# Performance work log

Measured on AMD Instinct MI355X. Metric: run time of the kernel, lower is better.

Reference implementation:

```python
import jax, jax.numpy as jnp
import numpy as np

CA, CZ, CS, CSI = 128, 128, 384, 256
NH, HD, NB, A = 8, 16, 6, 7
RMAX, SMAX = 32, 2
RELP_DIM = 4 * (RMAX + 1) + 1 + 2 * (SMAX + 1)  # 139


def make_relp(L):
    # single-chain relative-position features: [L, L, 139]
    i = jnp.arange(L)
    d = i[:, None] - i[None, :]
    a_rel_pos = jax.nn.one_hot(jnp.clip(d + RMAX, 0, 2 * RMAX), 2 * (RMAX + 1))
    d_tok = jnp.where(d == 0, RMAX, 2 * RMAX + 1)  # same-res only on diagonal
    a_rel_tok = jax.nn.one_hot(d_tok, 2 * (RMAX + 1))
    same_ent = jnp.ones((L, L, 1), jnp.float32)
    a_rel_chain = jax.nn.one_hot(jnp.full((L, L), SMAX), 2 * (SMAX + 1))
    return jnp.concatenate([a_rel_pos, a_rel_tok, same_ent, a_rel_chain], axis=-1)


def ln(x, g, b):
    m = x.mean(-1, keepdims=True)
    v = ((x - m) ** 2).mean(-1, keepdims=True)
    return (x - m) / jnp.sqrt(v + 1e-5) * g + b


def setup_inputs():
    key = jax.random.key(0)
    ks = iter(jax.random.split(key, 64))
    def p(*shape):
        return (jax.random.normal(next(ks), shape, jnp.float32) * 0.05)
    B, Ns, L = 1, 2, 384
    inp = dict(
        x_t=jax.random.normal(next(ks), (B, Ns, L, A, 3), jnp.float32),
        sigma=jax.random.uniform(next(ks), (B, Ns), jnp.float32),
        s_inputs=jax.random.normal(next(ks), (B, L, CSI), jnp.float32),
        s_trunk=jax.random.normal(next(ks), (B, L, CS), jnp.float32),
        z_trunk=jax.random.normal(next(ks), (B, L, L, CZ), jnp.float32),
        token_mask=jnp.ones((B, L), bool),
        s_in_w=p(CSI, CS), s_in_b=p(CS),
        relp_w=p(RELP_DIM, CZ), relp_b=p(CZ),
        t1_w=p(1, CS), t1_b=p(CS), t2_w=p(CS, CS), t2_b=p(CS),
        xp_w=p(3 * A, CA), xp_b=p(CA),
        s2a_w=p(CS, CA), s2a_b=p(CA),
        out_w=p(CA, 3 * A), out_b=p(3 * A),
        an_g=jnp.ones((NB, CA)), an_b=jnp.zeros((NB, CA)),
        zn_g=jnp.ones((NB, CZ)), zn_b=jnp.zeros((NB, CZ)),
        qw=p(NB, CA, CA), qb=p(NB, CA),
        kw=p(NB, CA, CA), kb=p(NB, CA),
        vw=p(NB, CA, CA), vb=p(NB, CA),
        zw=p(NB, CZ, NH), zb=p(NB, NH),
        ow=p(NB, CA, CA), ob=p(NB, CA),
        f1w=p(NB, CA, 4 * CA), f1b=p(NB, 4 * CA),
        f2w=p(NB, 4 * CA, CA), f2b=p(NB, CA),
    )
    return inp


def reference(x_t, sigma, s_inputs, s_trunk, z_trunk, token_mask,
              s_in_w, s_in_b, relp_w, relp_b, t1_w, t1_b, t2_w, t2_b,
              xp_w, xp_b, s2a_w, s2a_b, out_w, out_b,
              an_g, an_b, zn_g, zn_b, qw, qb, kw, kb, vw, vb,
              zw, zb, ow, ob, f1w, f1b, f2w, f2b):
    B, Ns, L = x_t.shape[:3]
    relp = make_relp(L)                                   # [L, L, 139]
    pair_z = z_trunk + relp @ relp_w + relp_b             # [B, L, L, CZ]
    s_cond = s_trunk + s_inputs @ s_in_w + s_in_b         # [B, L, CS]
    t_feat = jax.nn.silu(sigma.reshape(B * Ns, 1) @ t1_w + t1_b) @ t2_w + t2_b
    single_s = s_cond[:, None] + t_feat.reshape(B, Ns, CS)[:, :, None]  # [B,Ns,L,CS]
    a = x_t.reshape(B, Ns, L, 3 * A) @ xp_w + xp_b + single_s @ s2a_w + s2a_b
    a2 = a.reshape(B * Ns, L, CA)
    z2 = jnp.broadcast_to(pair_z[:, None], (B, Ns, L, L, CZ)).reshape(B * Ns, L, L, CZ)
    m = jnp.broadcast_to(token_mask[:, None], (B, Ns, L)).reshape(B * Ns, L)
    pair_mask = m[:, :, None] & m[:, None, :]             # [B*Ns, L, L]
    scale = 1.0 / np.sqrt(HD).astype(np.float32)
    for i in range(NB):
        an = ln(a2, an_g[i], an_b[i])
        zn = ln(z2, zn_g[i], zn_b[i])
        q = (an @ qw[i] + qb[i]).reshape(-1, L, NH, HD)
        k = (an @ kw[i] + kb[i]).reshape(-1, L, NH, HD)
        v = (an @ vw[i] + vb[i]).reshape(-1, L, NH, HD)
        logits = jnp.einsum('blhd,bmhd->bhlm', q, k) * scale
        bias = (zn @ zw[i] + zb[i]).transpose(0, 3, 1, 2)  # [B*Ns, NH, L, L]
        logits = jnp.where(pair_mask[:, None], logits + bias, -1e9)
        attn = jax.nn.softmax(logits, axis=-1)
        o = jnp.einsum('bhlm,bmhd->blhd', attn, v).reshape(-1, L, CA)
        a2 = a2 + (o @ ow[i] + ob[i])
        an2 = ln(a2, an_g[i], an_b[i])
        a2 = a2 + jax.nn.gelu(an2 @ f1w[i] + f1b[i], approximate=False) @ f2w[i] + f2b[i]
    vout = (a2 @ out_w + out_b).reshape(B, Ns, L, A, 3)
    return vout * token_mask[:, None, :, None, None].astype(vout.dtype)
```

## Files before the change

### kernel.cpp

```cpp
#include <hip/hip_runtime.h>
#include <math.h>

#define L 384
#define CA 128
#define NH 8
#define HD 16
#define NB 6
#define NS 2
#define NP (L*L)

typedef __attribute__((ext_vector_type(4))) float f32x4;
typedef __attribute__((ext_vector_type(8))) short s16x8;
typedef __attribute__((ext_vector_type(4))) unsigned short u16x4;
typedef unsigned short ushort_t;

__device__ inline unsigned short f2bf(float f){
  union { float f; unsigned int u; } v; v.f = f;
  unsigned int u = v.u;
  unsigned int r = u + 0x7FFF + ((u>>16)&1);
  return (unsigned short)(r>>16);
}
__device__ inline float bf2f(ushort_t u){
  union { float f; unsigned int i; } v; v.i = ((unsigned int)u)<<16; return v.f;
}

#define WT_LAYER 196608

__global__ __launch_bounds__(256) void k_pre0(
    const float* zng, const float* znb, const float* zw, const float* zb,
    const float* relp_w, const float* relp_b,
    ushort_t* wzT, float* rbase, float* cb){
  int t = threadIdx.x;
  __shared__ float part[48][5];
  for(int idx=t; idx<6144; idx+=256){
    int h = idx>>7, c = idx&127;
    wzT[h*128+c] = f2bf(zng[(h>>3)*128+c]*zw[((h>>3)*128+c)*8+(h&7)]);
  }
  if(t<128) rbase[t] = relp_w[132*128+t] + relp_w[135*128+t] + relp_b[t];
  if(t<192){
    int h = t>>2, ch = t&3, blk = h>>3, hh = h&7;
    float acc = 0.f;
    #pragma unroll 8
    for(int c=ch*32; c<ch*32+32; c++)
      acc += znb[blk*128+c]*zw[(blk*128+c)*8+hh];
    part[h][ch] = acc;
  }
  __syncthreads();
  if(t<48) cb[t] = zb[t] + part[t][0]+part[t][1]+part[t][2]+part[t][3];
}

__global__ __launch_bounds__(256, 4) void k_mega(
    const float* z_trunk, const float* relp_w, const float* rbase,
    const ushort_t* wzT, const float* cb, ushort_t* bias_all,
    const float* qw, const float* kw, const float* vw,
    const float* f1w, const float* f2w, const float* ow,
    const float* s_in_w, const float* s2a_w,
    ushort_t* wT, ushort_t* s_in_wT, ushort_t* s2a_wT,
    const float* sigma, const float* t1w, const float* t1b,
    const float* t2w, const float* t2b, float* t_feat){
  __shared__ float smem[4160];
  int bid = blockIdx.x, t = threadIdx.x;

  if(bid < 2304){
    int lane = t&63, wv = t>>6;
    int rowf = lane&15, kg = lane>>4;
    int p0 = bid*64 + wv*16;
    int p = p0 + rowf;
    int i = p/L, j = p - i*L, d = i - j;
    int r1 = d+32; r1 = r1<0?0:(r1>64?64:r1);
    int r2 = (d==0) ? 98 : 131;
    const float* zp  = z_trunk + (size_t)p*128 + kg*8;

    f32x4 z0a = *(const f32x4*)(zp+  0), z0b = *(const f32x4*)(zp+  4);
    f32x4 z1a = *(const f32x4*)(zp+ 32), z1b = *(const f32x4*)(zp+ 36);
    f32x4 z2a = *(const f32x4*)(zp+ 64), z2b = *(const f32x4*)(zp+ 68);
    f32x4 z3a = *(const f32x4*)(zp+ 96), z3b = *(const f32x4*)(zp+100);

    const float* w1p = relp_w + r1*128 + kg*8;
    const float* w2p = relp_w + r2*128 + kg*8;
    const float* rbp = rbase + kg*8;
    f32x4 c0a = *(const f32x4*)(w1p+  0) + *(const f32x4*)(w2p+  0) + *(const f32x4*)(rbp+  0);
    f32x4 c0b = *(const f32x4*)(w1p+  4) + *(const f32x4*)(w2p+  4) + *(const f32x4*)(rbp+  4);
    f32x4 c1a = *(const f32x4*)(w1p+ 32) + *(const f32x4*)(w2p+ 32) + *(const f32x4*)(rbp+ 32);
    f32x4 c1b = *(const f32x4*)(w1p+ 36) + *(const f32x4*)(w2p+ 36) + *(const f32x4*)(rbp+ 36);
    f32x4 c2a = *(const f32x4*)(w1p+ 64) + *(const f32x4*)(w2p+ 64) + *(const f32x4*)(rbp+ 64);
    f32x4 c2b = *(const f32x4*)(w1p+ 68) + *(const f32x4*)(w2p+ 68) + *(const f32x4*)(rbp+ 68);
    f32x4 c3a = *(const f32x4*)(w1p+ 96) + *(const f32x4*)(w2p+ 96) + *(const f32x4*)(rbp+ 96);
    f32x4 c3b = *(const f32x4*)(w1p+100) + *(const f32x4*)(w2p+100) + *(const f32x4*)(rbp+100);

    float val[4][8];
    float s = 0.f;
    #pragma unroll
    for(int jj=0;jj<4;jj++){
      val[0][jj]   = z0a[jj]+c0a[jj];  val[0][jj+4] = z0b[jj]+c0b[jj];
      val[1][jj]   = z1a[jj]+c1a[jj];  val[1][jj+4] = z1b[jj]+c1b[jj];
      val[2][jj]   = z2a[jj]+c2a[jj];  val[2][jj+4] = z2b[jj]+c2b[jj];
      val[3][jj]   = z3a[jj]+c3a[jj];  val[3][jj+4] = z3b[jj]+c3b[jj];
    }
    #pragma unroll
    for(int ks=0;ks<4;ks++)
      #pragma unroll
      for(int jj=0;jj<8;jj++) s += val[ks][jj];
    s += __shfl_xor(s,16,64); s += __shfl_xor(s,32,64);
    float mean = s*(1.f/128.f);
    float q2 = 0.f;
    #pragma unroll
    for(int ks=0; ks<4; ks++)
      #pragma unroll
      for(int jj=0;jj<8;jj++){ float dd = val[ks][jj]-mean; q2 += dd*dd; }
    q2 += __shfl_xor(q2,16,64); q2 += __shfl_xor(q2,32,64);
    float rstd = rsqrtf(q2*(1.f/128.f) + 1e-5f);

    s16x8 af[4];
    #pragma unroll
    for(int ks=0; ks<4; ks++)
      #pragma unroll
      for(int jj=0;jj<8;jj++) af[ks][jj] = (short)f2bf((val[ks][jj]-mean)*rstd);

    float* myc = smem + wv*816;
    #pragma unroll
    for(int ht=0; ht<3; ht++){
      int col = ht*16 + rowf;
      float cbv = cb[col];
      f32x4 acc = {cbv,cbv,cbv,cbv};
      #pragma unroll
      for(int ks=0; ks<4; ks++){
        s16x8 bf = *(const s16x8*)&wzT[col*128 + ks*32 + kg*8];
        acc = __builtin_amdgcn_mfma_f32_16x16x32_bf16(af[ks], bf, acc, 0,0,0);
      }
      #pragma unroll
      for(int i2=0;i2<4;i2++) myc[col*17 + kg*4 + i2] = acc[i2];
    }
    int i0 = p0/L, qt_ = i0>>4, q16 = i0&15, j0 = p0 - i0*L;
    #pragma unroll
    for(int it=0; it<12; it++){
      int idx = lane + it*64;
      int pl = idx>>4, c = idx&15;
      int li_ = pl>>3, h_ = pl&7;
      bias_all[(size_t)((li_*24+qt_)*8+h_)*6144 + q16*384 + j0 + c] =
          f2bf(myc[pl*17 + c]);
    }
  } else if(bid < 2628){
    float (*tl)[65] = (float(*)[65])smem;
    int b = bid - 2304;
    const float* src; ushort_t* dst;
    int M, N, k0, n0;
    if(b < 96){
      int mat = b>>2, li = mat>>2, wsel = mat&3, tile = b&3;
      const float* const ws_[4] = {qw, kw, vw, ow};
      const int off_[4] = {0, 16384, 32768, 180224};
      src = ws_[wsel] + (size_t)li*16384;
      dst = wT + (size_t)li*WT_LAYER + off_[wsel];
      M = 128; N = 128; k0 = (tile>>1)*64; n0 = (tile&1)*64;
    } else if(b < 192){
      int idx = b-96, li = idx>>4, tile = idx&15;
      src = f1w + (size_t)li*65536;
      dst = wT + (size_t)li*WT_LAYER + 49152;
      M = 128; N = 512; k0 = (tile>>3)*64; n0 = (tile&7)*64;
    } else if(b < 288){
      int idx = b-192, li = idx>>4, tile = idx&15;
      src = f2w + (size_t)li*65536;
      dst = wT + (size_t)li*WT_LAYER + 114688;
      M = 512; N = 128; k0 = (tile>>1)*64; n0 = (tile&1)*64;
    } else if(b < 312){
      int tile = b-288;
      src = s_in_w; dst = s_in_wT;
      M = 256; N = 384; k0 = (tile/6)*64; n0 = (tile%6)*64;
    } else {
      int tile = b-312;
      src = s2a_w; dst = s2a_wT;
      M = 384; N = 128; k0 = (tile>>1)*64; n0 = (tile&1)*64;
    }
    float v[16];
    #pragma unroll
    for(int it=0;it<16;it++){
      int i = t + it*256;
      v[it] = src[(size_t)(k0+(i>>6))*N + n0+(i&63)];
    }
    #pragma unroll
    for(int it=0;it<16;it++){
      int i = t + it*256;
      tl[i>>6][i&63] = v[it];
    }
    __syncthreads();
    #pragma unroll
    for(int it=0;it<16;it++){
      int i = t + it*256;
      dst[(size_t)(n0+(i>>6))*M + k0+(i&63)] = f2bf(tl[i&63][i>>6]);
    }
  } else {
    int j = bid - 2628;
    int s = j/6, c0 = (j%6)*64;
    float sg = sigma[s];
    for(int i=t; i<384; i+=256){
      float x = sg*t1w[i] + t1b[i];
      smem[i] = x / (1.f + expf(-x));
    }
    __syncthreads();
    int col = c0 + (t&63), ch = t>>6;
    float acc = 0.f;
    #pragma unroll 8
    for(int k=ch*96; k<ch*96+96; k++)
      acc += smem[k]*t2w[(size_t)k*384+col];
    smem[384 + ch*64 + (t&63)] = acc;
    __syncthreads();
    if(t<64)
      t_feat[s*384 + c0 + t] = t2b[c0+t]
        + smem[384+t] + smem[448+t] + smem[512+t] + smem[576+t];
  }
}

__device__ inline void qkv_project(ushort_t zh[16][152], const ushort_t* wTl,
                                   const float* qb, const float* kb, const float* vb,
                                   ushort_t* q_bf, ushort_t* k_bf, ushort_t* vT_bf,
                                   int s_idx, int lbase, int wv, int rowf, int kg){
  s16x8 af[4];
  #pragma unroll
  for(int ks=0;ks<4;ks++) af[ks] = *(const s16x8*)&zh[rowf][ks*32 + kg*8];
  #pragma unroll
  for(int u=0;u<6;u++){
    int unit = wv*6 + u;
    int proj = unit>>3, nt = unit&7;
    int col = nt*16 + rowf;
    const ushort_t* wp = wTl + proj*16384;
    const float* bias = proj==0? qb : (proj==1? kb : vb);
    float bv = bias[col];
    f32x4 acc = {bv,bv,bv,bv};
    #pragma unroll
    for(int ks=0;ks<4;ks++){
      s16x8 bf = *(const s16x8*)&wp[col*128 + ks*32 + kg*8];
      acc = __builtin_amdgcn_mfma_f32_16x16x32_bf16(af[ks], bf, acc, 0,0,0);
    }
    int sh = s_idx*NH + nt;
    if(proj==2){
      #pragma unroll
      for(int i2=0;i2<4;i2++)
        vT_bf[((size_t)sh*16 + rowf)*384 + lbase + kg*4 + i2] = f2bf(acc[i2]);
    } else {
      float sc = (proj==0)? 0.25f : 1.0f;
      ushort_t* outp = (proj==0)? q_bf : k_bf;
      #pragma unroll
      for(int i2=0;i2<4;i2++)
        outp[((size_t)sh*384 + lbase + kg*4 + i2)*16 + rowf] = f2bf(acc[i2]*sc);
    }
  }
}

__global__ __launch_bounds__(256) void k_qkv0(
    const float* x_t, const float* s_inputs, const float* s_trunk,
    const float* s_in_b, const ushort_t* s_in_wT,
    const float* s2a_b, const ushort_t* s2a_wT,
    const float* xp_w, const float* xp_b, const float* t_feat,
    const float* g, const float* bb,
    const ushort_t* wTl, const float* qb, const float* kb, const float* vb,
    float* a2, ushort_t* q_bf, ushort_t* k_bf, ushort_t* vT_bf){
  __shared__ ushort_t si[16][280];
  __shared__ ushort_t scb[16][408];
  __shared__ float xrow[16][21];
  __shared__ float a_new[16][132];
  __shared__ ushort_t zh[16][152];
  int t = threadIdx.x, lane = t&63, wv = t>>6;
  int rowf = lane&15, kg = lane>>4;
  int bid = blockIdx.x, s_idx = bid/24, lt = bid%24;
  int lr0 = lt*16;

  for(int i=t;i<16*256;i+=256){
    int r=i>>8, c=i&255;
    si[r][c] = f2bf(s_inputs[(size_t)(lr0+r)*256+c]);
  }
  for(int i=t;i<16*21;i+=256){
    int r=i/21, u=i%21;
    xrow[r][u] = x_t[((size_t)s_idx*L + lr0 + r)*21 + u];
  }
  __syncthreads();

  {
    s16x8 af1[8];
    #pragma unroll
    for(int ks=0;ks<8;ks++) af1[ks] = *(const s16x8*)&si[rowf][ks*32+kg*8];
    const float* tf = t_feat + s_idx*384;
    #pragma unroll
    for(int nn=0;nn<6;nn++){
      int col = (wv*6+nn)*16 + rowf;
      float bv = s_in_b[col];
      f32x4 acc = {bv,bv,bv,bv};
      #pragma unroll
      for(int ks=0;ks<8;ks++){
        s16x8 bf = *(const s16x8*)&s_in_wT[col*256 + ks*32 + kg*8];
        acc = __builtin_amdgcn_mfma_f32_16x16x32_bf16(af1[ks], bf, acc, 0,0,0);
      }
      float tfc = tf[col];
      #pragma unroll
      for(int i2=0;i2<4;i2++){
        int r = kg*4+i2;
        scb[r][col] = f2bf(acc[i2] + s_trunk[(size_t)(lr0+r)*384+col] + tfc);
      }
    }
  }
  __syncthreads();

  {
    s16x8 xf[12];
    #pragma unroll
    for(int ks=0;ks<12;ks++) xf[ks] = *(const s16x8*)&scb[rowf][ks*32+kg*8];
    #pragma unroll
    for(int nn=0;nn<2;nn++){
      int col = (wv*2+nn)*16 + rowf;
      float base = xp_b[col] + s2a_b[col];
      f32x4 acc;
      #pragma unroll
      for(int i2=0;i2<4;i2++){
        float xc = base;
        #pragma unroll
        for(int u=0;u<21;u++) xc += xrow[kg*4+i2][u]*xp_w[u*128+col];
        acc[i2] = xc;
      }
      #pragma unroll
      for(int ks=0;ks<12;ks++){
        s16x8 bf = *(const s16x8*)&s2a_wT[col*384 + ks*32 + kg*8];
        acc = __builtin_amdgcn_mfma_f32_16x16x32_bf16(xf[ks], bf, acc, 0,0,0);
      }
      #pragma unroll
      for(int i2=0;i2<4;i2++){
        int r = kg*4+i2;
        a_new[r][col] = acc[i2];
        a2[((size_t)(s_idx*L + lr0 + r))*128 + col] = acc[i2];
      }
    }
  }
  __syncthreads();

  {
    int row = t>>4, sub = t&15;
    const float* xp = &a_new[row][sub*8];
    f32x4 x0 = *(const f32x4*)xp;
    f32x4 x1 = *(const f32x4*)(xp+4);
    float s = x0[0]+x0[1]+x0[2]+x0[3]+x1[0]+x1[1]+x1[2]+x1[3];
    s += __shfl_xor(s,1,64); s += __shfl_xor(s,2,64);
    s += __shfl_xor(s,4,64); s += __shfl_xor(s,8,64);
    float mean = s*(1.f/128.f);
    float q2 = 0.f;
    #pragma unroll
    for(int jj=0;jj<4;jj++){ float d0=x0[jj]-mean, d1=x1[jj]-mean; q2 += d0*d0+d1*d1; }
    q2 += __shfl_xor(q2,1,64); q2 += __shfl_xor(q2,2,64);
    q2 += __shfl_xor(q2,4,64); q2 += __shfl_xor(q2,8,64);
    float rstd = rsqrtf(q2*(1.f/128.f)+1e-5f);
    int c0 = sub*8;
    f32x4 g0 = *(const f32x4*)(g+c0), g1 = *(const f32x4*)(g+c0+4);
    f32x4 b0 = *(const f32x4*)(bb+c0), b1 = *(const f32x4*)(bb+c0+4);
    s16x8 pack;
    #pragma unroll
    for(int jj=0;jj<4;jj++){
      pack[jj]   = (short)f2bf((x0[jj]-mean)*rstd*g0[jj]+b0[jj]);
      pack[jj+4] = (short)f2bf((x1[jj]-mean)*rstd*g1[jj]+b1[jj]);
    }
    *(s16x8*)&zh[row][c0] = pack;
  }
  __syncthreads();
  qkv_project(zh, wTl, qb, kb, vb, q_bf, k_bf, vT_bf, s_idx, lr0, wv, rowf, kg);
}

__global__ __launch_bounds__(1024) void k_fused(
    float* a2, const float* an_g, const float* an_b, const ushort_t* wT,
    const float* qb_all, const float* kb_all, const float* vb_all,
    const float* ob_all, const float* f1b_all, const float* f2b_all,
    ushort_t* q_bf, ushort_t* k_bf, ushort_t* vT_bf,
    const ushort_t* bias_all, const float* out_w, const float* out_b,
    float* out, int li){
  __shared__ float orow[16][132];
  __shared__ float ocomb[8][16][20];
  __shared__ float lcomb[8][16];
  union SM {
    struct {
      ushort_t biasw[16][16][200];
      ushort_t P[16][16][72];
    } fl;
    struct {
      float a_new[16][132];
      ushort_t zh[16][152];
      ushort_t h_lds[16][536];
      float fcomb[8][16][20];
    } post;
  };
  __shared__ SM sm;

  int t = threadIdx.x, lane = t&63, wv = t>>6;
  int rowf = lane&15, kg = lane>>4;
  int bid = blockIdx.x, s_idx = bid/24, qt = bid%24;
  int r0 = bid*16;
  const ushort_t* wTl = wT + (size_t)li*WT_LAYER;
  const float* g  = an_g + li*128;
  const float* bb = an_b + li*128;

  {
    int h = wv>>1, kh = wv&1;
    int sh = s_idx*NH + h;
    {
      const ushort_t* btile = bias_all + (size_t)(li*24+qt)*8*6144
                            + (size_t)h*16*384 + kh*192;
      #pragma unroll
      for(int it=0; it<6; it++){
        int idx = lane + it*64;
        int row = idx/24, seg = idx%24;
        *(s16x8*)&sm.fl.biasw[wv][row][seg*8] =
            *(const s16x8*)&btile[(size_t)row*384 + seg*8];
      }
    }
    ushort_t (*Pw)[72] = sm.fl.P[wv];
    s16x8 qf = {0,0,0,0,0,0,0,0};
    if(kg < 2) qf = *(const s16x8*)&q_bf[((size_t)sh*384 + qt*16 + rowf)*16 + kg*8];
    const ushort_t* kp = k_bf + (size_t)sh*384*16;
    const ushort_t* vp = vT_bf + ((size_t)sh*16 + rowf)*384;

    f32x4 o0 = {0,0,0,0}, o1 = {0,0,0,0};
    float l_acc = 0.f;

    s16x8 kfc[4];
    #pragma unroll
    for(int t4=0;t4<4;t4++){
      kfc[t4] = (s16x8){0,0,0,0,0,0,0,0};
      if(kg < 2) kfc[t4] = *(const s16x8*)&kp[((size_t)(kh*192 + t4*16 + rowf))*16 + kg*8];
    }

    #pragma unroll
    for(int c=0;c<3;c++){
      int key0 = kh*192 + c*64;
      s16x8 vbf0 = *(const s16x8*)&vp[key0 + kg*8];
      s16x8 vbf1 = *(const s16x8*)&vp[key0 + 32 + kg*8];
      s16x8 kfn[4];
      if(c < 2){
        #pragma unroll
        for(int t4=0;t4<4;t4++){
          kfn[t4] = (s16x8){0,0,0,0,0,0,0,0};
          if(kg < 2) kfn[t4] = *(const s16x8*)&kp[((size_t)(key0 + 64 + t4*16 + rowf))*16 + kg*8];
        }
      }
      f32x4 st[4];
      #pragma unroll
      for(int t4=0;t4<4;t4++){
        u16x4 bb4 = *(const u16x4*)&sm.fl.biasw[wv][rowf][c*64 + t4*16 + kg*4];
        f32x4 cin;
        #pragma unroll
        for(int jj=0;jj<4;jj++) cin[jj] = bf2f(bb4[jj]);
        st[t4] = __builtin_amdgcn_mfma_f32_16x16x32_bf16(kfc[t4], qf, cin, 0,0,0);
      }
      #pragma unroll
      for(int t4=0;t4<4;t4++){
        float p0 = __expf(st[t4][0]), p1 = __expf(st[t4][1]);
        float p2 = __expf(st[t4][2]), p3 = __expf(st[t4][3]);
        l_acc += (p0+p1)+(p2+p3);
        u16x4 pk = {f2bf(p0), f2bf(p1), f2bf(p2), f2bf(p3)};
        *(u16x4*)&Pw[rowf][t4*16 + kg*4] = pk;
      }
      {
        s16x8 pa = *(const s16x8*)&Pw[rowf][kg*8];
        o0 = __builtin_amdgcn_mfma_f32_16x16x32_bf16(pa, vbf0, o0, 0,0,0);
        s16x8 pb = *(const s16x8*)&Pw[rowf][32 + kg*8];
        o1 = __builtin_amdgcn_mfma_f32_16x16x32_bf16(pb, vbf1, o1, 0,0,0);
      }
      if(c < 2){
        #pragma unroll
        for(int t4=0;t4<4;t4++) kfc[t4] = kfn[t4];
      }
    }
    f32x4 o_acc = o0 + o1;
    l_acc += __shfl_xor(l_acc, 16, 64);
    l_acc += __shfl_xor(l_acc, 32, 64);
    if(kh==1){
      #pragma unroll
      for(int i2=0;i2<4;i2++) ocomb[h][kg*4+i2][rowf] = o_acc[i2];
      if(kg==0) lcomb[h][rowf] = l_acc;
    }
    __syncthreads();
    if(kh==0){
      l_acc += lcomb[h][rowf];
      #pragma unroll
      for(int i2=0;i2<4;i2++) o_acc[i2] += ocomb[h][kg*4+i2][rowf];
      float inv = 1.f / l_acc;
      #pragma unroll
      for(int i2=0;i2<4;i2++){
        float invq = __shfl(inv, kg*4 + i2, 64);
        orow[kg*4+i2][h*16 + rowf] = o_acc[i2]*invq;
      }
    }
  }
  __syncthreads();

  if(wv < 8){
    s16x8 af[4];
    #pragma unroll
    for(int ks=0;ks<4;ks++){
      f32x4 v0 = *(const f32x4*)&orow[rowf][ks*32+kg*8];
      f32x4 v1 = *(const f32x4*)&orow[rowf][ks*32+kg*8+4];
      s16x8 p;
      #pragma unroll
      for(int jj=0;jj<4;jj++){ p[jj] = (short)f2bf(v0[jj]); p[jj+4] = (short)f2bf(v1[jj]); }
      af[ks] = p;
    }
    const ushort_t* wo = wTl + 180224;
    const float* obp = ob_all + li*128;
    int col = wv*16 + rowf;
    float bv = obp[col];
    f32x4 acc = {bv,bv,bv,bv};
    f32x4 accB = {0,0,0,0};
    #pragma unroll
    for(int ks=0;ks<2;ks++){
      s16x8 bf = *(const s16x8*)&wo[col*128 + ks*32 + kg*8];
      acc = __builtin_amdgcn_mfma_f32_16x16x32_bf16(af[ks], bf, acc, 0,0,0);
      s16x8 bf2 = *(const s16x8*)&wo[col*128 + (ks+2)*32 + kg*8];
      accB = __builtin_amdgcn_mfma_f32_16x16x32_bf16(af[ks+2], bf2, accB, 0,0,0);
    }
    acc += accB;
    #pragma unroll
    for(int i2=0;i2<4;i2++){
      int r = kg*4+i2;
      sm.post.a_new[r][col] = a2[(size_t)(r0+r)*128 + col] + acc[i2];
    }
  }
  __syncthreads();

  {
    int row = wv, c0 = lane*2;
    float x0 = sm.post.a_new[row][c0], x1 = sm.post.a_new[row][c0+1];
    float s = x0+x1;
    s += __shfl_xor(s,1,64); s += __shfl_xor(s,2,64); s += __shfl_xor(s,4,64);
    s += __shfl_xor(s,8,64); s += __shfl_xor(s,16,64); s += __shfl_xor(s,32,64);
    float mean = s*(1.f/128.f);
    float d0=x0-mean, d1=x1-mean;
    float q2 = d0*d0+d1*d1;
    q2 += __shfl_xor(q2,1,64); q2 += __shfl_xor(q2,2,64); q2 += __shfl_xor(q2,4,64);
    q2 += __shfl_xor(q2,8,64); q2 += __shfl_xor(q2,16,64); q2 += __shfl_xor(q2,32,64);
    float rstd = rsqrtf(q2*(1.f/128.f)+1e-5f);
    unsigned int pk = (unsigned int)f2bf(d0*rstd*g[c0]+bb[c0])
                    | ((unsigned int)f2bf(d1*rstd*g[c0+1]+bb[c0+1])<<16);
    *(unsigned int*)&sm.post.zh[row][c0] = pk;
  }
  __syncthreads();

  {
    s16x8 xf[4];
    #pragma unroll
    for(int ks=0;ks<4;ks++) xf[ks] = *(const s16x8*)&sm.post.zh[rowf][ks*32 + kg*8];
    const ushort_t* w1 = wTl + 49152;
    const float* f1bp = f1b_all + li*512;
    #pragma unroll
    for(int nn=0; nn<2; nn++){
      int col = (wv*2+nn)*16 + rowf;
      float bv = f1bp[col];
      f32x4 acc = {bv,bv,bv,bv};
      #pragma unroll
      for(int ks=0;ks<4;ks++){
        s16x8 bf = *(const s16x8*)&w1[col*128 + ks*32 + kg*8];
        acc = __builtin_amdgcn_mfma_f32_16x16x32_bf16(xf[ks], bf, acc, 0,0,0);
      }
      #pragma unroll
      for(int i2=0;i2<4;i2++){
        float x = acc[i2];
        float ge = 0.5f*x*(1.f + erff(x*0.70710678f));
        sm.post.h_lds[kg*4+i2][col] = f2bf(ge);
      }
    }
  }
  __syncthreads();

  {
    const ushort_t* w2 = wTl + 114688;
    const float* f2bp = f2b_all + li*128;
    int ct = wv>>1, kh2 = wv&1;
    int col2 = ct*16 + rowf;
    float bv = kh2? 0.f : f2bp[col2];
    f32x4 accA = {bv,bv,bv,bv};
    f32x4 accB = {0,0,0,0};
    int ks0 = kh2*8;
    #pragma unroll
    for(int kk=0; kk<4; kk++){
      s16x8 hfA = *(const s16x8*)&sm.post.h_lds[rowf][(ks0+kk)*32 + kg*8];
      s16x8 bfA = *(const s16x8*)&w2[col2*512 + (ks0+kk)*32 + kg*8];
      accA = __builtin_amdgcn_mfma_f32_16x16x32_bf16(hfA, bfA, accA, 0,0,0);
      s16x8 hfB = *(const s16x8*)&sm.post.h_lds[rowf][(ks0+kk+4)*32 + kg*8];
      s16x8 bfB = *(const s16x8*)&w2[col2*512 + (ks0+kk+4)*32 + kg*8];
      accB = __builtin_amdgcn_mfma_f32_16x16x32_bf16(hfB, bfB, accB, 0,0,0);
    }
    accA += accB;
    if(kh2==1){
      #pragma unroll
      for(int i2=0;i2<4;i2++) sm.post.fcomb[ct][kg*4+i2][rowf] = accA[i2];
    }
    __syncthreads();
    if(kh2==0){
      #pragma unroll
      for(int i2=0;i2<4;i2++){
        int r = kg*4+i2;
        float fin = sm.post.a_new[r][col2] + accA[i2] + sm.post.fcomb[ct][r][rowf];
        a2[(size_t)(r0+r)*128 + col2] = fin;
        sm.post.a_new[r][col2] = fin;
      }
    }
  }
  __syncthreads();

  if(li < NB-1){
    const float* g2  = an_g + (li+1)*128;
    const float* bb2 = an_b + (li+1)*128;
    {
      int row = wv, c0 = lane*2;
      float x0 = sm.post.a_new[row][c0], x1 = sm.post.a_new[row][c0+1];
      float s = x0+x1;
      s += __shfl_xor(s,1,64); s += __shfl_xor(s,2,64); s += __shfl_xor(s,4,64);
      s += __shfl_xor(s,8,64); s += __shfl_xor(s,16,64); s += __shfl_xor(s,32,64);
      float mean = s*(1.f/128.f);
      float d0=x0-mean, d1=x1-mean;
      float q2 = d0*d0+d1*d1;
      q2 += __shfl_xor(q2,1,64); q2 += __shfl_xor(q2,2,64); q2 += __shfl_xor(q2,4,64);
      q2 += __shfl_xor(q2,8,64); q2 += __shfl_xor(q2,16,64); q2 += __shfl_xor(q2,32,64);
      float rstd = rsqrtf(q2*(1.f/128.f)+1e-5f);
      unsigned int pk = (unsigned int)f2bf(d0*rstd*g2[c0]+bb2[c0])
                      | ((unsigned int)f2bf(d1*rstd*g2[c0+1]+bb2[c0+1])<<16);
      *(unsigned int*)&sm.post.zh[row][c0] = pk;
    }
    __syncthreads();
    {
      const ushort_t* wTn = wT + (size_t)(li+1)*WT_LAYER;
      const float* qb2 = qb_all + (li+1)*128;
      const float* kb2 = kb_all + (li+1)*128;
      const float* vb2 = vb_all + (li+1)*128;
      s16x8 af[4];
      #pragma unroll
      for(int ks=0;ks<4;ks++) af[ks] = *(const s16x8*)&sm.post.zh[rowf][ks*32 + kg*8];
      #pragma unroll
      for(int u=0;u<2;u++){
        int unit = wv + u*16;
        if(unit < 24){
          int proj = unit>>3, nt = unit&7;
          int col = nt*16 + rowf;
          const ushort_t* wp = wTn + proj*16384;
          const float* bias = proj==0? qb2 : (proj==1? kb2 : vb2);
          float bv = bias[col];
          f32x4 acc = {bv,bv,bv,bv};
          #pragma unroll
          for(int ks=0;ks<4;ks++){
            s16x8 bf = *(const s16x8*)&wp[col*128 + ks*32 + kg*8];
            acc = __builtin_amdgcn_mfma_f32_16x16x32_bf16(af[ks], bf, acc, 0,0,0);
          }
          int sh = s_idx*NH + nt;
          if(proj==2){
            #pragma unroll
            for(int i2=0;i2<4;i2++)
              vT_bf[((size_t)sh*16 + rowf)*384 + qt*16 + kg*4 + i2] = f2bf(acc[i2]);
          } else {
            float sc = (proj==0)? 0.25f : 1.0f;
            ushort_t* outp = (proj==0)? q_bf : k_bf;
            #pragma unroll
            for(int i2=0;i2<4;i2++)
              outp[((size_t)sh*384 + qt*16 + kg*4 + i2)*16 + rowf] = f2bf(acc[i2]*sc);
          }
        }
      }
    }
  } else {
    for(int idx=t; idx<336; idx+=1024){
      int r = idx/21, c = idx%21;
      float acc = out_b[c];
      #pragma unroll 8
      for(int kk=0;kk<128;kk++) acc += sm.post.a_new[r][kk]*out_w[kk*21+c];
      out[(size_t)(r0+r)*21 + c] = acc;
    }
  }
}

extern "C" void kernel_launch(void* const* d_in, const int* in_sizes, int n_in,
                              void* d_out, int out_size, void* d_ws, size_t ws_size,
                              hipStream_t stream){
  const float* x_t      = (const float*)d_in[0];
  const float* sigma    = (const float*)d_in[1];
  const float* s_inputs = (const float*)d_in[2];
  const float* s_trunk  = (const float*)d_in[3];
  const float* z_trunk  = (const float*)d_in[4];
  const float* s_in_w = (const float*)d_in[6];
  const float* s_in_b = (const float*)d_in[7];
  const float* relp_w = (const float*)d_in[8];
  const float* relp_b = (const float*)d_in[9];
  const float* t1_w = (const float*)d_in[10];
  const float* t1_b = (const float*)d_in[11];
  const float* t2_w = (const float*)d_in[12];
  const float* t2_b = (const float*)d_in[13];
  const float* xp_w = (const float*)d_in[14];
  const float* xp_b = (const float*)d_in[15];
  const float* s2a_w = (const float*)d_in[16];
  const float* s2a_b = (const float*)d_in[17];
  const float* out_w = (const float*)d_in[18];
  const float* out_b = (const float*)d_in[19];
  const float* an_g = (const float*)d_in[20];
  const float* an_b = (const float*)d_in[21];
  const float* zn_g = (const float*)d_in[22];
  const float* zn_b = (const float*)d_in[23];
  const float* qw = (const float*)d_in[24];
  const float* qb = (const float*)d_in[25];
  const float* kw = (const float*)d_in[26];
  const float* kb = (const float*)d_in[27];
  const float* vw = (const float*)d_in[28];
  const float* vb = (const float*)d_in[29];
  const float* zw = (const float*)d_in[30];
  const float* zb = (const float*)d_in[31];
  const float* ow = (const float*)d_in[32];
  const float* ob = (const float*)d_in[33];
  const float* f1w = (const float*)d_in[34];
  const float* f1b = (const float*)d_in[35];
  const float* f2w = (const float*)d_in[36];
  const float* f2b = (const float*)d_in[37];

  float* ws = (float*)d_ws;
  ushort_t* bias_all = (ushort_t*)ws;
  float* cb     = ws + (size_t)24*NP;
  float* t_feat = cb + 48;
  float* a2     = t_feat + 768;
  float* rbase  = a2 + (size_t)NS*L*CA;
  ushort_t* wT      = (ushort_t*)(rbase + 128);
  ushort_t* wzT     = wT + (size_t)6*WT_LAYER;
  ushort_t* q_bf    = wzT + 6144;
  ushort_t* k_bf    = q_bf + 98304;
  ushort_t* vT_bf   = k_bf + 98304;
  ushort_t* s_in_wT = vT_bf + 98304;
  ushort_t* s2a_wT  = s_in_wT + 98304;
  float* outp = (float*)d_out;

  k_pre0<<<1,256,0,stream>>>(zn_g,zn_b,zw,zb,relp_w,relp_b,wzT,rbase,cb);
  k_mega<<<2640,256,0,stream>>>(z_trunk,relp_w,rbase,wzT,cb,bias_all,
                                qw,kw,vw,f1w,f2w,ow,s_in_w,s2a_w,
                                wT,s_in_wT,s2a_wT,
                                sigma,t1_w,t1_b,t2_w,t2_b,t_feat);
  k_qkv0<<<48,256,0,stream>>>(x_t,s_inputs,s_trunk,s_in_b,s_in_wT,
                              s2a_b,s2a_wT,xp_w,xp_b,t_feat,
                              an_g, an_b, wT, qb, kb, vb,
                              a2, q_bf, k_bf, vT_bf);
  for(int i=0;i<NB;i++){
    k_fused<<<48,1024,0,stream>>>(a2, an_g, an_b, wT,
        qb, kb, vb, ob, f1b, f2b,
        q_bf, k_bf, vT_bf, bias_all,
        out_w, out_b, outp, i);
  }
}
```

Measured before the change: 198.8 us.

## Reorder mega-kernel blocks and prefetch weight fragments ahead of barriers

The mega kernel now dispatches the weight-transpose and time-embedding blocks first, so these short latency-bound tasks are not queued behind the 2304 pair-bias blocks. The time-embedding work is split across twice as many blocks to spread out its dependent loop. In the fused layer kernel, the out-projection, FFN1, FFN2 and next-layer QKV weight fragments are loaded into registers before the preceding __syncthreads, so global load latency overlaps the barrier wait, and some barriers are removed or moved. The cost is higher register pressure in a 1024-thread block, which may cause spills.

```diff
diff --git a/kernel.cpp b/kernel.cpp
--- a/kernel.cpp
+++ b/kernel.cpp
@@ -61,88 +61,9 @@
   __shared__ float smem[4160];
   int bid = blockIdx.x, t = threadIdx.x;
 
-  if(bid < 2304){
-    int lane = t&63, wv = t>>6;
-    int rowf = lane&15, kg = lane>>4;
-    int p0 = bid*64 + wv*16;
-    int p = p0 + rowf;
-    int i = p/L, j = p - i*L, d = i - j;
-    int r1 = d+32; r1 = r1<0?0:(r1>64?64:r1);
-    int r2 = (d==0) ? 98 : 131;
-    const float* zp  = z_trunk + (size_t)p*128 + kg*8;
-
-    f32x4 z0a = *(const f32x4*)(zp+  0), z0b = *(const f32x4*)(zp+  4);
-    f32x4 z1a = *(const f32x4*)(zp+ 32), z1b = *(const f32x4*)(zp+ 36);
-    f32x4 z2a = *(const f32x4*)(zp+ 64), z2b = *(const f32x4*)(zp+ 68);
-    f32x4 z3a = *(const f32x4*)(zp+ 96), z3b = *(const f32x4*)(zp+100);
-
-    const float* w1p = relp_w + r1*128 + kg*8;
-    const float* w2p = relp_w + r2*128 + kg*8;
-    const float* rbp = rbase + kg*8;
-    f32x4 c0a = *(const f32x4*)(w1p+  0) + *(const f32x4*)(w2p+  0) + *(const f32x4*)(rbp+  0);
-    f32x4 c0b = *(const f32x4*)(w1p+  4) + *(const f32x4*)(w2p+  4) + *(const f32x4*)(rbp+  4);
-    f32x4 c1a = *(const f32x4*)(w1p+ 32) + *(const f32x4*)(w2p+ 32) + *(const f32x4*)(rbp+ 32);
-    f32x4 c1b = *(const f32x4*)(w1p+ 36) + *(const f32x4*)(w2p+ 36) + *(const f32x4*)(rbp+ 36);
-    f32x4 c2a = *(const f32x4*)(w1p+ 64) + *(const f32x4*)(w2p+ 64) + *(const f32x4*)(rbp+ 64);
-    f32x4 c2b = *(const f32x4*)(w1p+ 68) + *(const f32x4*)(w2p+ 68) + *(const f32x4*)(rbp+ 68);
-    f32x4 c3a = *(const f32x4*)(w1p+ 96) + *(const f32x4*)(w2p+ 96) + *(const f32x4*)(rbp+ 96);
-    f32x4 c3b = *(const f32x4*)(w1p+100) + *(const f32x4*)(w2p+100) + *(const f32x4*)(rbp+100);
-
-    float val[4][8];
-    float s = 0.f;
-    #pragma unroll
-    for(int jj=0;jj<4;jj++){
-      val[0][jj]   = z0a[jj]+c0a[jj];  val[0][jj+4] = z0b[jj]+c0b[jj];
-      val[1][jj]   = z1a[jj]+c1a[jj];  val[1][jj+4] = z1b[jj]+c1b[jj];
-      val[2][jj]   = z2a[jj]+c2a[jj];  val[2][jj+4] = z2b[jj]+c2b[jj];
-      val[3][jj]   = z3a[jj]+c3a[jj];  val[3][jj+4] = z3b[jj]+c3b[jj];
-    }
-    #pragma unroll
-    for(int ks=0;ks<4;ks++)
-      #pragma unroll
-      for(int jj=0;jj<8;jj++) s += val[ks][jj];
-    s += __shfl_xor(s,16,64); s += __shfl_xor(s,32,64);
-    float mean = s*(1.f/128.f);
-    float q2 = 0.f;
-    #pragma unroll
-    for(int ks=0; ks<4; ks++)
-      #pragma unroll
-      for(int jj=0;jj<8;jj++){ float dd = val[ks][jj]-mean; q2 += dd*dd; }
-    q2 += __shfl_xor(q2,16,64); q2 += __shfl_xor(q2,32,64);
-    float rstd = rsqrtf(q2*(1.f/128.f) + 1e-5f);
-
-    s16x8 af[4];
-    #pragma unroll
-    for(int ks=0; ks<4; ks++)
-      #pragma unroll
-      for(int jj=0;jj<8;jj++) af[ks][jj] = (short)f2bf((val[ks][jj]-mean)*rstd);
-
-    float* myc = smem + wv*816;
-    #pragma unroll
-    for(int ht=0; ht<3; ht++){
-      int col = ht*16 + rowf;
-      float cbv = cb[col];
-      f32x4 acc = {cbv,cbv,cbv,cbv};
-      #pragma unroll
-      for(int ks=0; ks<4; ks++){
-        s16x8 bf = *(const s16x8*)&wzT[col*128 + ks*32 + kg*8];
-        acc = __builtin_amdgcn_mfma_f32_16x16x32_bf16(af[ks], bf, acc, 0,0,0);
-      }
-      #pragma unroll
-      for(int i2=0;i2<4;i2++) myc[col*17 + kg*4 + i2] = acc[i2];
-    }
-    int i0 = p0/L, qt_ = i0>>4, q16 = i0&15, j0 = p0 - i0*L;
-    #pragma unroll
-    for(int it=0; it<12; it++){
-      int idx = lane + it*64;
-      int pl = idx>>4, c = idx&15;
-      int li_ = pl>>3, h_ = pl&7;
-      bias_all[(size_t)((li_*24+qt_)*8+h_)*6144 + q16*384 + j0 + c] =
-          f2bf(myc[pl*17 + c]);
-    }
-  } else if(bid < 2628){
+  if(bid < 324){
     float (*tl)[65] = (float(*)[65])smem;
-    int b = bid - 2304;
+    int b = bid;
     const float* src; ushort_t* dst;
     int M, N, k0, n0;
     if(b < 96){
@@ -188,25 +109,108 @@
       int i = t + it*256;
       dst[(size_t)(n0+(i>>6))*M + k0+(i&63)] = f2bf(tl[i&63][i>>6]);
     }
-  } else {
-    int j = bid - 2628;
-    int s = j/6, c0 = (j%6)*64;
+  } else if(bid < 348){
+    int j = bid - 324;
+    int s = j/12, c0 = (j%12)*32;
     float sg = sigma[s];
     for(int i=t; i<384; i+=256){
       float x = sg*t1w[i] + t1b[i];
       smem[i] = x / (1.f + expf(-x));
     }
     __syncthreads();
-    int col = c0 + (t&63), ch = t>>6;
+    int col = c0 + (t&31), ch = t>>5;
     float acc = 0.f;
     #pragma unroll 8
-    for(int k=ch*96; k<ch*96+96; k++)
+    for(int k=ch*48; k<ch*48+48; k++)
       acc += smem[k]*t2w[(size_t)k*384+col];
-    smem[384 + ch*64 + (t&63)] = acc;
+    smem[384 + ch*32 + (t&31)] = acc;
     __syncthreads();
-    if(t<64)
-      t_feat[s*384 + c0 + t] = t2b[c0+t]
-        + smem[384+t] + smem[448+t] + smem[512+t] + smem[576+t];
+    if(t<32){
+      float r = t2b[c0+t];
+      #pragma unroll
+      for(int c=0;c<8;c++) r += smem[384 + c*32 + t];
+      t_feat[s*384 + c0 + t] = r;
+    }
+  } else {
+    int pb = bid - 348;
+    int lane = t&63, wv = t>>6;
+    int rowf = lane&15, kg = lane>>4;
+    int p0 = pb*64 + wv*16;
+    int p = p0 + rowf;
+    int i = p/L, j = p - i*L, d = i - j;
+    int r1 = d+32; r1 = r1<0?0:(r1>64?64:r1);
+    int r2 = (d==0) ? 98 : 131;
+    const float* zp  = z_trunk + (size_t)p*128 + kg*8;
+
+    f32x4 z0a = *(const f32x4*)(zp+  0), z0b = *(const f32x4*)(zp+  4);
+    f32x4 z1a = *(const f32x4*)(zp+ 32), z1b = *(const f32x4*)(zp+ 36);
+    f32x4 z2a = *(const f32x4*)(zp+ 64), z2b = *(const f32x4*)(zp+ 68);
+    f32x4 z3a = *(const f32x4*)(zp+ 96), z3b = *(const f32x4*)(zp+100);
+
+    const float* w1p = relp_w + r1*128 + kg*8;
+    const float* w2p = relp_w + r2*128 + kg*8;
+    const float* rbp = rbase + kg*8;
+    f32x4 c0a = *(const f32x4*)(w1p+  0) + *(const f32x4*)(w2p+  0) + *(const f32x4*)(rbp+  0);
+    f32x4 c0b = *(const f32x4*)(w1p+  4) + *(const f32x4*)(w2p+  4) + *(const f32x4*)(rbp+  4);
+    f32x4 c1a = *(const f32x4*)(w1p+ 32) + *(const f32x4*)(w2p+ 32) + *(const f32x4*)(rbp+ 32);
+    f32x4 c1b = *(const f32x4*)(w1p+ 36) + *(const f32x4*)(w2p+ 36) + *(const f32x4*)(rbp+ 36);
+    f32x4 c2a = *(const f32x4*)(w1p+ 64) + *(const f32x4*)(w2p+ 64) + *(const f32x4*)(rbp+ 64);
+    f32x4 c2b = *(const f32x4*)(w1p+ 68) + *(const f32x4*)(w2p+ 68) + *(const f32x4*)(rbp+ 68);
+    f32x4 c3a = *(const f32x4*)(w1p+ 96) + *(const f32x4*)(w2p+ 96) + *(const f32x4*)(rbp+ 96);
+    f32x4 c3b = *(const f32x4*)(w1p+100) + *(const f32x4*)(w2p+100) + *(const f32x4*)(rbp+100);
+
+    float val[4][8];
+    float s = 0.f;
+    #pragma unroll
+    for(int jj=0;jj<4;jj++){
+      val[0][jj]   = z0a[jj]+c0a[jj];  val[0][jj+4] = z0b[jj]+c0b[jj];
+      val[1][jj]   = z1a[jj]+c1a[jj];  val[1][jj+4] = z1b[jj]+c1b[jj];
+      val[2][jj]   = z2a[jj]+c2a[jj];  val[2][jj+4] = z2b[jj]+c2b[jj];
+      val[3][jj]   = z3a[jj]+c3a[jj];  val[3][jj+4] = z3b[jj]+c3b[jj];
+    }
+    #pragma unroll
+    for(int ks=0;ks<4;ks++)
+      #pragma unroll
+      for(int jj=0;jj<8;jj++) s += val[ks][jj];
+    s += __shfl_xor(s,16,64); s += __shfl_xor(s,32,64);
+    float mean = s*(1.f/128.f);
+    float q2 = 0.f;
+    #pragma unroll
+    for(int ks=0; ks<4; ks++)
+      #pragma unroll
+      for(int jj=0;jj<8;jj++){ float dd = val[ks][jj]-mean; q2 += dd*dd; }
+    q2 += __shfl_xor(q2,16,64); q2 += __shfl_xor(q2,32,64);
+    float rstd = rsqrtf(q2*(1.f/128.f) + 1e-5f);
+
+    s16x8 af[4];
+    #pragma unroll
+    for(int ks=0; ks<4; ks++)
+      #pragma unroll
+      for(int jj=0;jj<8;jj++) af[ks][jj] = (short)f2bf((val[ks][jj]-mean)*rstd);
+
+    float* myc = smem + wv*816;
+    #pragma unroll
+    for(int ht=0; ht<3; ht++){
+      int col = ht*16 + rowf;
+      float cbv = cb[col];
+      f32x4 acc = {cbv,cbv,cbv,cbv};
+      #pragma unroll
+      for(int ks=0; ks<4; ks++){
+        s16x8 bf = *(const s16x8*)&wzT[col*128 + ks*32 + kg*8];
+        acc = __builtin_amdgcn_mfma_f32_16x16x32_bf16(af[ks], bf, acc, 0,0,0);
+      }
+      #pragma unroll
+      for(int i2=0;i2<4;i2++) myc[col*17 + kg*4 + i2] = acc[i2];
+    }
+    int i0 = p0/L, qt_ = i0>>4, q16 = i0&15, j0 = p0 - i0*L;
+    #pragma unroll
+    for(int it=0; it<12; it++){
+      int idx = lane + it*64;
+      int pl = idx>>4, c = idx&15;
+      int li_ = pl>>3, h_ = pl&7;
+      bias_all[(size_t)((li_*24+qt_)*8+h_)*6144 + q16*384 + j0 + c] =
+          f2bf(myc[pl*17 + c]);
+    }
   }
 }
 
@@ -484,6 +488,15 @@
       }
     }
   }
+
+  s16x8 wof[4];
+  {
+    const ushort_t* wo = wTl + 180224;
+    int col = (wv&7)*16 + rowf;
+    #pragma unroll
+    for(int ks=0;ks<4;ks++)
+      wof[ks] = *(const s16x8*)&wo[col*128 + ks*32 + kg*8];
+  }
   __syncthreads();
 
   if(wv < 8){
@@ -497,7 +510,6 @@
       for(int jj=0;jj<4;jj++){ p[jj] = (short)f2bf(v0[jj]); p[jj+4] = (short)f2bf(v1[jj]); }
       af[ks] = p;
     }
-    const ushort_t* wo = wTl + 180224;
     const float* obp = ob_all + li*128;
     int col = wv*16 + rowf;
     float bv = obp[col];
@@ -505,16 +517,26 @@
     f32x4 accB = {0,0,0,0};
     #pragma unroll
     for(int ks=0;ks<2;ks++){
-      s16x8 bf = *(const s16x8*)&wo[col*128 + ks*32 + kg*8];
-      acc = __builtin_amdgcn_mfma_f32_16x16x32_bf16(af[ks], bf, acc, 0,0,0);
-      s16x8 bf2 = *(const s16x8*)&wo[col*128 + (ks+2)*32 + kg*8];
-      accB = __builtin_amdgcn_mfma_f32_16x16x32_bf16(af[ks+2], bf2, accB, 0,0,0);
+      acc  = __builtin_amdgcn_mfma_f32_16x16x32_bf16(af[ks],   wof[ks],   acc,  0,0,0);
+      accB = __builtin_amdgcn_mfma_f32_16x16x32_bf16(af[ks+2], wof[ks+2], accB, 0,0,0);
     }
     acc += accB;
     #pragma unroll
     for(int i2=0;i2<4;i2++){
       int r = kg*4+i2;
       sm.post.a_new[r][col] = a2[(size_t)(r0+r)*128 + col] + acc[i2];
+    }
+  }
+
+  s16x8 w1f[2][4];
+  {
+    const ushort_t* w1 = wTl + 49152;
+    #pragma unroll
+    for(int nn=0; nn<2; nn++){
+      int col = (wv*2+nn)*16 + rowf;
+      #pragma unroll
+      for(int ks=0;ks<4;ks++)
+        w1f[nn][ks] = *(const s16x8*)&w1[col*128 + ks*32 + kg*8];
     }
   }
   __syncthreads();
@@ -541,7 +563,6 @@
     s16x8 xf[4];
     #pragma unroll
     for(int ks=0;ks<4;ks++) xf[ks] = *(const s16x8*)&sm.post.zh[rowf][ks*32 + kg*8];
-    const ushort_t* w1 = wTl + 49152;
     const float* f1bp = f1b_all + li*512;
     #pragma unroll
     for(int nn=0; nn<2; nn++){
@@ -549,10 +570,8 @@
       float bv = f1bp[col];
       f32x4 acc = {bv,bv,bv,bv};
       #pragma unroll
-      for(int ks=0;ks<4;ks++){
-        s16x8 bf = *(const s16x8*)&w1[col*128 + ks*32 + kg*8];
-        acc = __builtin_amdgcn_mfma_f32_16x16x32_bf16(xf[ks], bf, acc, 0,0,0);
-      }
+      for(int ks=0;ks<4;ks++)
+        acc = __builtin_amdgcn_mfma_f32_16x16x32_bf16(xf[ks], w1f[nn][ks], acc, 0,0,0);
       #pragma unroll
       for(int i2=0;i2<4;i2++){
         float x = acc[i2];
@@ -561,12 +580,21 @@
       }
     }
   }
-  __syncthreads();
-
+
+  s16x8 w2f[8];
+  int ct = wv>>1, kh2 = wv&1;
   {
     const ushort_t* w2 = wTl + 114688;
+    int col2 = ct*16 + rowf;
+    int ks0 = kh2*8;
+    #pragma unroll
+    for(int kk=0; kk<8; kk++)
+      w2f[kk] = *(const s16x8*)&w2[col2*512 + (ks0+kk)*32 + kg*8];
+  }
+  __syncthreads();
+
+  {
     const float* f2bp = f2b_all + li*128;
-    int ct = wv>>1, kh2 = wv&1;
     int col2 = ct*16 + rowf;
     float bv = kh2? 0.f : f2bp[col2];
     f32x4 accA = {bv,bv,bv,bv};
@@ -575,11 +603,9 @@
     #pragma unroll
     for(int kk=0; kk<4; kk++){
       s16x8 hfA = *(const s16x8*)&sm.post.h_lds[rowf][(ks0+kk)*32 + kg*8];
-      s16x8 bfA = *(const s16x8*)&w2[col2*512 + (ks0+kk)*32 + kg*8];
-      accA = __builtin_amdgcn_mfma_f32_16x16x32_bf16(hfA, bfA, accA, 0,0,0);
+      accA = __builtin_amdgcn_mfma_f32_16x16x32_bf16(hfA, w2f[kk], accA, 0,0,0);
       s16x8 hfB = *(const s16x8*)&sm.post.h_lds[rowf][(ks0+kk+4)*32 + kg*8];
-      s16x8 bfB = *(const s16x8*)&w2[col2*512 + (ks0+kk+4)*32 + kg*8];
-      accB = __builtin_amdgcn_mfma_f32_16x16x32_bf16(hfB, bfB, accB, 0,0,0);
+      accB = __builtin_amdgcn_mfma_f32_16x16x32_bf16(hfB, w2f[kk+4], accB, 0,0,0);
     }
     accA += accB;
     if(kh2==1){
@@ -597,9 +623,26 @@
       }
     }
   }
-  __syncthreads();
 
   if(li < NB-1){
+    s16x8 qkf[2][4];
+    {
+      const ushort_t* wTn = wT + (size_t)(li+1)*WT_LAYER;
+      #pragma unroll
+      for(int u=0;u<2;u++){
+        int unit = wv + u*16;
+        if(unit < 24){
+          int proj = unit>>3, nt = unit&7;
+          int col = nt*16 + rowf;
+          const ushort_t* wp = wTn + proj*16384;
+          #pragma unroll
+          for(int ks=0;ks<4;ks++)
+            qkf[u][ks] = *(const s16x8*)&wp[col*128 + ks*32 + kg*8];
+        }
+      }
+    }
+    __syncthreads();
+
     const float* g2  = an_g + (li+1)*128;
     const float* bb2 = an_b + (li+1)*128;
     {
@@ -620,7 +663,6 @@
     }
     __syncthreads();
     {
-      const ushort_t* wTn = wT + (size_t)(li+1)*WT_LAYER;
       const float* qb2 = qb_all + (li+1)*128;
       const float* kb2 = kb_all + (li+1)*128;
       const float* vb2 = vb_all + (li+1)*128;
@@ -633,15 +675,12 @@
         if(unit < 24){
           int proj = unit>>3, nt = unit&7;
           int col = nt*16 + rowf;
-          const ushort_t* wp = wTn + proj*16384;
           const float* bias = proj==0? qb2 : (proj==1? kb2 : vb2);
           float bv = bias[col];
           f32x4 acc = {bv,bv,bv,bv};
           #pragma unroll
-          for(int ks=0;ks<4;ks++){
-            s16x8 bf = *(const s16x8*)&wp[col*128 + ks*32 + kg*8];
-            acc = __builtin_amdgcn_mfma_f32_16x16x32_bf16(af[ks], bf, acc, 0,0,0);
-          }
+          for(int ks=0;ks<4;ks++)
+            acc = __builtin_amdgcn_mfma_f32_16x16x32_bf16(af[ks], qkf[u][ks], acc, 0,0,0);
           int sh = s_idx*NH + nt;
           if(proj==2){
             #pragma unroll
@@ -658,6 +697,7 @@
       }
     }
   } else {
+    __syncthreads();
     for(int idx=t; idx<336; idx+=1024){
       int r = idx/21, c = idx%21;
       float acc = out_b[c];
@@ -725,7 +765,7 @@
   float* outp = (float*)d_out;
 
   k_pre0<<<1,256,0,stream>>>(zn_g,zn_b,zw,zb,relp_w,relp_b,wzT,rbase,cb);
-  k_mega<<<2640,256,0,stream>>>(z_trunk,relp_w,rbase,wzT,cb,bias_all,
+  k_mega<<<2652,256,0,stream>>>(z_trunk,relp_w,rbase,wzT,cb,bias_all,
                                 qw,kw,vw,f1w,f2w,ow,s_in_w,s2a_w,
                                 wT,s_in_wT,s2a_wT,
                                 sigma,t1_w,t1_b,t2_w,t2_b,t_feat);
```

New measurement: 209.9 us. 1.06x slower.
